# Kernel optimization log

Hardware: AMD Instinct MI355X
Metric: run time of the kernel (lower is better)

The kernel has to match this reference:

```python
import jax, jax.numpy as jnp
import numpy as np

B, S, D, H = 32, 128, 64, 4
HD = D // H            # head dim 16
HT = 4 * D             # hidden_t_dim = 256
TE = 4 * HT            # time_embed_dim = 1024
V = 1024               # vocab
STEP = 0.1             # step_size (Lie-Trotter step)


def setup_inputs():
    key = jax.random.key(0)
    ks = jax.random.split(key, 12)
    n = lambda k, shp: 0.02 * jax.random.normal(k, shp, jnp.float32)
    return dict(
        inputs_idx=jax.random.randint(ks[0], (B, S), 0, V),
        num_loops=100,
        wte=n(ks[1], (V, D)),
        wpe=n(ks[2], (S, D)),
        t_w1=n(ks[3], (HT, TE)), t_b1=jnp.zeros((TE,), jnp.float32),
        t_w2=n(ks[4], (TE, D)), t_b2=jnp.zeros((D,), jnp.float32),
        ln1_g=jnp.ones((D,), jnp.float32), ln1_b=jnp.zeros((D,), jnp.float32),
        w_qkv=n(ks[5], (D, 3 * D)), b_qkv=jnp.zeros((3 * D,), jnp.float32),
        w_o=n(ks[6], (D, D)), b_o=jnp.zeros((D,), jnp.float32),
        ln2_g=jnp.ones((D,), jnp.float32), ln2_b=jnp.zeros((D,), jnp.float32),
        w_fc=n(ks[7], (D, 4 * D)), b_fc=jnp.zeros((4 * D,), jnp.float32),
        w_pr=n(ks[8], (4 * D, D)), b_pr=jnp.zeros((D,), jnp.float32),
        lnf_g=jnp.ones((D,), jnp.float32), lnf_b=jnp.zeros((D,), jnp.float32),
    )


def _ln(x, g, b, eps=1e-5):
    mu = jnp.mean(x, axis=-1, keepdims=True)
    var = jnp.var(x, axis=-1, keepdims=True)
    return (x - mu) * jax.lax.rsqrt(var + eps) * g + b


def _timestep_embedding(t, dim):
    # sinusoidal (diffusion-style) embedding of scalar step index t -> (dim,)
    half = dim // 2
    freqs = jnp.exp(-np.log(10000.0) * jnp.arange(half, dtype=jnp.float32) / half)
    args = t * freqs
    return jnp.concatenate([jnp.cos(args), jnp.sin(args)], axis=-1)


def reference(inputs_idx, num_loops, wte, wpe, t_w1, t_b1, t_w2, t_b2,
              ln1_g, ln1_b, w_qkv, b_qkv, w_o, b_o,
              ln2_g, ln2_b, w_fc, b_fc, w_pr, b_pr, lnf_g, lnf_b):
    x = wte[inputs_idx] + wpe[jnp.arange(S)]          # (B,S,D)
    neg_inf = jnp.float32(-1e9)
    cmask = jnp.where(jnp.tril(jnp.ones((S, S), bool)), 0.0, neg_inf)  # causal
    scale = 1.0 / np.sqrt(HD)

    def step(x, t):
        # shared time embedding added to state each loop iteration
        te = _timestep_embedding(t, HT)
        temb = jax.nn.silu(te @ t_w1 + t_b1) @ t_w2 + t_b2   # (D,)
        x = x + temb
        # pre-norm attention, Lie-Trotter sub-step
        h = _ln(x, ln1_g, ln1_b)
        qkv = h @ w_qkv + b_qkv                               # (B,S,3D)
        q, k, v = jnp.split(qkv, 3, axis=-1)
        q = q.reshape(B, S, H, HD)
        k = k.reshape(B, S, H, HD)
        v = v.reshape(B, S, H, HD)
        att = jnp.einsum('bqhd,bkhd->bhqk', q, k) * scale + cmask
        att = jax.nn.softmax(att, axis=-1)
        a = jnp.einsum('bhqk,bkhd->bqhd', att, v).reshape(B, S, D)
        x = x + STEP * (a @ w_o + b_o)
        # pre-norm MLP, second sub-step
        h = _ln(x, ln2_g, ln2_b)
        m = jax.nn.gelu(h @ w_fc + b_fc) @ w_pr + b_pr
        x = x + STEP * m
        return x, None

    ts = jnp.arange(num_loops, dtype=jnp.float32)
    x, _ = jax.lax.scan(step, x, ts)
    return _ln(x, lnf_g, lnf_b)
```

## Files before the change

kernel.cpp:

```cpp
#include <hip/hip_runtime.h>
#include <hip/hip_bf16.h>
#include <math.h>

#define BB   32
#define SS   128
#define DD   64
#define HTT  256
#define TEE  1024
#define NTHR 1024
#define STEPF 0.1f

typedef __attribute__((ext_vector_type(8))) short short8b;
typedef __attribute__((ext_vector_type(4))) float float4v;

__device__ __forceinline__ unsigned short f2b(float f) {
    union { float f; unsigned int u; } x; x.f = f;
    unsigned int u = x.u + 0x7FFFu + ((x.u >> 16) & 1u);
    return (unsigned short)(u >> 16);
}
__device__ __forceinline__ unsigned int pack2(float lo, float hi) {
    return (unsigned int)f2b(lo) | ((unsigned int)f2b(hi) << 16);
}

__global__ void pack_frags(const float* __restrict__ w_qkv,
                           const float* __restrict__ w_o,
                           const float* __restrict__ w_fc,
                           const float* __restrict__ w_pr,
                           unsigned short* __restrict__ frags) {
    const int tile = blockIdx.x;
    const int t = threadIdx.x;
    const int lane = t >> 3, e = t & 7;
    const float* W; int N, nt, ks;
    if (tile < 24)      { W = w_qkv; N = 192; int s = tile;      nt = s >> 1; ks = s & 1; }
    else if (tile < 32) { W = w_o;   N = 64;  int s = tile - 24; nt = s >> 1; ks = s & 1; }
    else if (tile < 64) { W = w_fc;  N = 256; int s = tile - 32; nt = s >> 1; ks = s & 1; }
    else                { W = w_pr;  N = 64;  int s = tile - 64; nt = s >> 3; ks = s & 7; }
    const int k   = ks * 32 + (lane >> 4) * 8 + e;
    const int col = nt * 16 + (lane & 15);
    frags[tile * 512 + lane * 8 + e] = f2b(W[k * N + col]);
}

__global__ void temb_precompute(const int* __restrict__ nloops_p,
                                const float* __restrict__ t_w1,
                                const float* __restrict__ t_b1,
                                const float* __restrict__ t_w2,
                                const float* __restrict__ t_b2,
                                float* __restrict__ tembBuf) {
    const int t = blockIdx.x;
    const int nl = nloops_p[0];
    if (t >= nl) return;

    __shared__ float te_s[HTT];
    __shared__ float h1[TEE];
    const int tid = threadIdx.x;
    const float tf = (float)t;

    {
        int fi = (tid < 128) ? tid : (tid - 128);
        float freq = expf(-9.210340371976184f * (float)fi * (1.0f / 128.0f));
        float arg = tf * freq;
        te_s[tid] = (tid < 128) ? cosf(arg) : sinf(arg);
    }
    __syncthreads();

    for (int j = tid; j < TEE; j += 256) {
        float acc = t_b1[j];
        for (int i = 0; i < HTT; ++i)
            acc = fmaf(te_s[i], t_w1[i * TEE + j], acc);
        h1[j] = acc / (1.0f + expf(-acc));
    }
    __syncthreads();

    {
        const int d = tid >> 2, part = tid & 3;
        float acc = 0.0f;
        for (int j = part; j < TEE; j += 4)
            acc = fmaf(h1[j], t_w2[j * DD + d], acc);
        acc += __shfl_xor(acc, 1);
        acc += __shfl_xor(acc, 2);
        if (part == 0) tembBuf[t * DD + d] = acc + t_b2[d];
    }
}

__device__ __forceinline__ float gelu_tanh(float u) {
    float z = 0.7978845608028654f * (u + 0.044715f * u * u * u);
    float e = __expf(2.0f * z);
    float th = 1.0f - 2.0f / (e + 1.0f);
    return 0.5f * u * (1.0f + th);
}

__global__ __launch_bounds__(NTHR, 4)
void looped_tf(const int* __restrict__ idx,
               const int* __restrict__ nloops_p,
               const float* __restrict__ wte,
               const float* __restrict__ wpe,
               const float* __restrict__ ln1_g, const float* __restrict__ ln1_b,
               const float* __restrict__ b_qkv,
               const float* __restrict__ b_o,
               const float* __restrict__ ln2_g, const float* __restrict__ ln2_b,
               const float* __restrict__ b_fc,
               const float* __restrict__ b_pr,
               const float* __restrict__ lnf_g, const float* __restrict__ lnf_b,
               const float* __restrict__ tembBuf,
               const unsigned short* __restrict__ frags,
               float* __restrict__ out) {
    __shared__ __align__(16) unsigned short hsb[SS * DD];
    __shared__ __align__(16) unsigned char pool[66560];
    __shared__ __align__(16) unsigned char pstage[16 * 2 * 1152];
    __shared__ __align__(16) unsigned short wfrag[16384];
    __shared__ __align__(16) float2 lnred[SS][2];

    unsigned char* qb  = pool;
    unsigned char* kb  = pool + 24576;
    unsigned char* vtb = pool + 49152;
    unsigned short* msb = (unsigned short*)pool;

    const unsigned short* fcF = frags + 32 * 512;
    const unsigned short* prF = frags + 64 * 512;

    const int b   = blockIdx.x;
    const int tid = threadIdx.x;
    const int nl  = nloops_p[0];
    const int wv  = tid >> 6;
    const int wg  = wv & 7;
    const int wh  = wv >> 3;
    const int ln  = tid & 63;
    const int fr  = ln & 15;
    const int fq  = ln >> 4;
    const int rowbase = wg * 16 + fq * 4;

    for (int i = tid; i < 2048; i += NTHR)
        ((int4*)wfrag)[i] = ((const int4*)frags)[i];

    float bqkvr[6], bfcr[8], bor[2], bprr[2];
    float l1g[2], l1b[2], l2g[2], l2b[2], lfg[2], lfb[2];
#pragma unroll
    for (int i = 0; i < 6; ++i) bqkvr[i] = b_qkv[(wh * 6 + i) * 16 + fr];
#pragma unroll
    for (int i = 0; i < 8; ++i) bfcr[i] = b_fc[(wh * 8 + i) * 16 + fr];
#pragma unroll
    for (int nc = 0; nc < 2; ++nc) {
        int c = (wh * 2 + nc) * 16 + fr;
        bor[nc] = b_o[c];  bprr[nc] = b_pr[c];
        l1g[nc] = ln1_g[c]; l1b[nc] = ln1_b[c];
        l2g[nc] = ln2_g[c]; l2b[nc] = ln2_b[c];
        lfg[nc] = lnf_g[c]; lfb[nc] = lnf_b[c];
    }

    float xr[4][2];
#pragma unroll
    for (int r = 0; r < 4; ++r) {
        int row = rowbase + r;
        int iv = idx[b * SS + row];
#pragma unroll
        for (int nc = 0; nc < 2; ++nc) {
            int c = (wh * 2 + nc) * 16 + fr;
            xr[r][nc] = wte[iv * 64 + c] + wpe[row * 64 + c];
        }
    }
    __syncthreads();

    auto ln_fused = [&](const float* g2, const float* b2) {
        float s1[4], s2[4];
#pragma unroll
        for (int r = 0; r < 4; ++r) {
            s1[r] = xr[r][0] + xr[r][1];
            s2[r] = xr[r][0]*xr[r][0] + xr[r][1]*xr[r][1];
        }
#pragma unroll
        for (int m = 1; m <= 8; m <<= 1) {
#pragma unroll
            for (int r = 0; r < 4; ++r) {
                s1[r] += __shfl_xor(s1[r], m);
                s2[r] += __shfl_xor(s2[r], m);
            }
        }
        if (fr == 0) {
#pragma unroll
            for (int r = 0; r < 4; ++r) {
                float2 v; v.x = s1[r]; v.y = s2[r];
                lnred[rowbase + r][wh] = v;
            }
        }
        __syncthreads();
#pragma unroll
        for (int r = 0; r < 4; ++r) {
            float2 oth = lnred[rowbase + r][wh ^ 1];
            float t1 = s1[r] + oth.x, t2 = s2[r] + oth.y;
            float mu = t1 * (1.0f / 64.0f);
            float var = t2 * (1.0f / 64.0f) - mu * mu;
            float rs = rsqrtf(var + 1e-5f);
            int row = rowbase + r;
            int swz = (row & 7) << 4;
#pragma unroll
            for (int nc = 0; nc < 2; ++nc) {
                float h = (xr[r][nc] - mu) * rs * g2[nc] + b2[nc];
                int byte = (row * 128 + ((wh * 2 + nc) * 16 + fr) * 2) ^ swz;
                *(unsigned short*)((char*)hsb + byte) = f2b(h);
            }
        }
        __syncthreads();
    };

    auto load_afrag = [&](const unsigned short* buf, int rstrideB, int kstep) -> short8b {
        int row = wg * 16 + fr;
        int byte = row * rstrideB + kstep * 64 + fq * 16;
        return *(const short8b*)((const char*)buf + (byte ^ ((row & 7) << 4)));
    };

    if (nl > 0) {
#pragma unroll
        for (int nc = 0; nc < 2; ++nc) {
            float tv = tembBuf[(wh * 2 + nc) * 16 + fr];
#pragma unroll
            for (int r = 0; r < 4; ++r) xr[r][nc] += tv;
        }
        ln_fused(l1g, l1b);
    }

    for (int t = 0; t < nl; ++t) {
        {
            short8b a0 = load_afrag(hsb, 128, 0);
            short8b a1 = load_afrag(hsb, 128, 1);
            float4v acc[6];
#pragma unroll
            for (int i = 0; i < 6; ++i) acc[i] = (float4v)0.0f;
#pragma unroll
            for (int i = 0; i < 6; ++i) {
                int nt = wh * 6 + i;
                short8b b0 = *(const short8b*)(&wfrag[(nt * 2 + 0) * 512 + ln * 8]);
                short8b b1 = *(const short8b*)(&wfrag[(nt * 2 + 1) * 512 + ln * 8]);
                acc[i] = __builtin_amdgcn_mfma_f32_16x16x32_bf16(a0, b0, acc[i], 0, 0, 0);
                acc[i] = __builtin_amdgcn_mfma_f32_16x16x32_bf16(a1, b1, acc[i], 0, 0, 0);
            }
#pragma unroll
            for (int i = 0; i < 6; ++i) {
                int nt = wh * 6 + i;
#pragma unroll
                for (int r = 0; r < 4; ++r) {
                    int row = rowbase + r;
                    unsigned short bv = f2b(acc[i][r] + bqkvr[i]);
                    if (nt < 4) {
                        int byte = nt * 6144 + row * 48 + fr * 2;
                        byte ^= ((row >> 3) & 7) << 4;
                        *(unsigned short*)(qb + byte) = bv;
                    } else if (nt < 8) {
                        int h = nt - 4;
                        int p = (row >> 1) + 64 * (row & 1);
                        *(unsigned short*)(kb + h * 6144 + p * 48 + fr * 2) = bv;
                    } else {
                        int h = nt - 8;
                        *(unsigned short*)(vtb + h * 4352 + fr * 272 + row * 2) = bv;
                    }
                }
            }
        }
        __syncthreads();

        {
            const bool lo = (ln < 32);
            short8b aq[2];
#pragma unroll
            for (int hh = 0; hh < 2; ++hh) {
                int h = wh * 2 + hh;
                short8b z = (short8b)(short)0;
                if (lo) {
                    int q = wg + 8 * fr;
                    int byte = h * 6144 + q * 48 + (fq & 1) * 16;
                    byte ^= (fr & 7) << 4;
                    z = *(const short8b*)(qb + byte);
                }
                aq[hh] = z;
            }
            short8b onesb;
#pragma unroll
            for (int e = 0; e < 8; ++e) onesb[e] = (short)0x3F80;

            float4v o[2], lac[2];
#pragma unroll
            for (int hh = 0; hh < 2; ++hh) { o[hh] = (float4v)0.0f; lac[hh] = (float4v)0.0f; }

            for (int ktp = 0; ktp < 4; ++ktp) {
#pragma unroll
                for (int hh = 0; hh < 2; ++hh) {
                    int h = wh * 2 + hh;
                    unsigned char* pst = pstage + (wv * 2 + hh) * 1152;
                    short8b bk0 = (short8b)(short)0, bk1 = (short8b)(short)0;
                    if (lo) {
                        int kbase = h * 6144 + (fq & 1) * 16;
                        bk0 = *(const short8b*)(kb + kbase + (ktp * 16 + fr) * 48);
                        bk1 = *(const short8b*)(kb + kbase + (64 + ktp * 16 + fr) * 48);
                    }
                    float4v s0 = __builtin_amdgcn_mfma_f32_16x16x32_bf16(aq[hh], bk0, (float4v)0.0f, 0, 0, 0);
                    float4v s1 = __builtin_amdgcn_mfma_f32_16x16x32_bf16(aq[hh], bk1, (float4v)0.0f, 0, 0, 0);
#pragma unroll
                    for (int r = 0; r < 4; ++r) {
                        int j = 4 * fq + r;
                        int q = wg + 8 * j;
                        int k0 = ktp * 32 + 2 * fr;
                        float p0 = (k0     <= q) ? __expf(s0[r] * 0.25f) : 0.0f;
                        float p1 = (k0 + 1 <= q) ? __expf(s1[r] * 0.25f) : 0.0f;
                        *(unsigned int*)(pst + j * 72 + fr * 4) = pack2(p0, p1);
                    }
                    short8b ap = *(const short8b*)(pst + fr * 72 + fq * 16);
                    short8b bv = *(const short8b*)(vtb + h * 4352 + fr * 272 + ktp * 64 + fq * 16);
                    o[hh]   = __builtin_amdgcn_mfma_f32_16x16x32_bf16(ap, bv, o[hh], 0, 0, 0);
                    lac[hh] = __builtin_amdgcn_mfma_f32_16x16x32_bf16(ap, onesb, lac[hh], 0, 0, 0);
                }
            }
#pragma unroll
            for (int hh = 0; hh < 2; ++hh) {
                int h = wh * 2 + hh;
#pragma unroll
                for (int r = 0; r < 4; ++r) {
                    int j = 4 * fq + r;
                    int q = wg + 8 * j;
                    float val = o[hh][r] / lac[hh][r];
                    int byte = (q * 128 + (h * 16 + fr) * 2) ^ ((q & 7) << 4);
                    *(unsigned short*)((char*)hsb + byte) = f2b(val);
                }
            }
        }
        __syncthreads();

        {
            short8b a0 = load_afrag(hsb, 128, 0);
            short8b a1 = load_afrag(hsb, 128, 1);
            float4v acc[2];
#pragma unroll
            for (int i = 0; i < 2; ++i) acc[i] = (float4v)0.0f;
#pragma unroll
            for (int i = 0; i < 2; ++i) {
                int nt = wh * 2 + i;
                short8b b0 = *(const short8b*)(&wfrag[(24 + nt * 2 + 0) * 512 + ln * 8]);
                short8b b1 = *(const short8b*)(&wfrag[(24 + nt * 2 + 1) * 512 + ln * 8]);
                acc[i] = __builtin_amdgcn_mfma_f32_16x16x32_bf16(a0, b0, acc[i], 0, 0, 0);
                acc[i] = __builtin_amdgcn_mfma_f32_16x16x32_bf16(a1, b1, acc[i], 0, 0, 0);
            }
#pragma unroll
            for (int i = 0; i < 2; ++i)
#pragma unroll
                for (int r = 0; r < 4; ++r)
                    xr[r][i] += STEPF * (acc[i][r] + bor[i]);
            ln_fused(l2g, l2b);
        }

        {
            short8b a0 = load_afrag(hsb, 128, 0);
            short8b a1 = load_afrag(hsb, 128, 1);
            float4v acc[8];
#pragma unroll
            for (int i = 0; i < 8; ++i) acc[i] = (float4v)0.0f;
#pragma unroll
            for (int i = 0; i < 8; ++i) {
                int nt = wh * 8 + i;
                short8b b0 = *(const short8b*)(fcF + ((nt * 2 + 0) * 64 + ln) * 8);
                short8b b1 = *(const short8b*)(fcF + ((nt * 2 + 1) * 64 + ln) * 8);
                acc[i] = __builtin_amdgcn_mfma_f32_16x16x32_bf16(a0, b0, acc[i], 0, 0, 0);
                acc[i] = __builtin_amdgcn_mfma_f32_16x16x32_bf16(a1, b1, acc[i], 0, 0, 0);
            }
            char* base = (char*)msb;
#pragma unroll
            for (int i = 0; i < 8; ++i) {
                int nt = wh * 8 + i;
#pragma unroll
                for (int r = 0; r < 4; ++r) {
                    int row = rowbase + r;
                    int byte = row * 512 + (nt * 16 + fr) * 2;
                    *(unsigned short*)(base + (byte ^ ((row & 7) << 4))) =
                        f2b(gelu_tanh(acc[i][r] + bfcr[i]));
                }
            }
        }
        __syncthreads();

        {
            short8b am[8];
#pragma unroll
            for (int ks = 0; ks < 8; ++ks)
                am[ks] = load_afrag(msb, 512, ks);
            float4v acc[2];
#pragma unroll
            for (int i = 0; i < 2; ++i) acc[i] = (float4v)0.0f;
#pragma unroll
            for (int i = 0; i < 2; ++i) {
                int nt = wh * 2 + i;
#pragma unroll
                for (int ks = 0; ks < 8; ++ks) {
                    short8b bp = *(const short8b*)(prF + ((nt * 8 + ks) * 64 + ln) * 8);
                    acc[i] = __builtin_amdgcn_mfma_f32_16x16x32_bf16(am[ks], bp, acc[i], 0, 0, 0);
                }
            }
#pragma unroll
            for (int i = 0; i < 2; ++i)
#pragma unroll
                for (int r = 0; r < 4; ++r)
                    xr[r][i] += STEPF * (acc[i][r] + bprr[i]);

            if (t + 1 < nl) {
#pragma unroll
                for (int nc = 0; nc < 2; ++nc) {
                    float tv = tembBuf[(t + 1) * 64 + (wh * 2 + nc) * 16 + fr];
#pragma unroll
                    for (int r = 0; r < 4; ++r) xr[r][nc] += tv;
                }
                ln_fused(l1g, l1b);
            }
        }
    }

    {
        float s1[4], s2[4];
#pragma unroll
        for (int r = 0; r < 4; ++r) {
            s1[r] = xr[r][0] + xr[r][1];
            s2[r] = xr[r][0]*xr[r][0] + xr[r][1]*xr[r][1];
        }
#pragma unroll
        for (int m = 1; m <= 8; m <<= 1) {
#pragma unroll
            for (int r = 0; r < 4; ++r) {
                s1[r] += __shfl_xor(s1[r], m);
                s2[r] += __shfl_xor(s2[r], m);
            }
        }
        if (fr == 0) {
#pragma unroll
            for (int r = 0; r < 4; ++r) {
                float2 v; v.x = s1[r]; v.y = s2[r];
                lnred[rowbase + r][wh] = v;
            }
        }
        __syncthreads();
#pragma unroll
        for (int r = 0; r < 4; ++r) {
            float2 oth = lnred[rowbase + r][wh ^ 1];
            float t1 = s1[r] + oth.x, t2 = s2[r] + oth.y;
            float mu = t1 * (1.0f / 64.0f);
            float var = t2 * (1.0f / 64.0f) - mu * mu;
            float rs = rsqrtf(var + 1e-5f);
            int row = rowbase + r;
#pragma unroll
            for (int nc = 0; nc < 2; ++nc) {
                int c = (wh * 2 + nc) * 16 + fr;
                out[b * SS * DD + row * 64 + c] = (xr[r][nc] - mu) * rs * lfg[nc] + lfb[nc];
            }
        }
    }
}

extern "C" void kernel_launch(void* const* d_in, const int* in_sizes, int n_in,
                              void* d_out, int out_size, void* d_ws, size_t ws_size,
                              hipStream_t stream) {
    const int*   idx    = (const int*)  d_in[0];
    const int*   nloops = (const int*)  d_in[1];
    const float* wte    = (const float*)d_in[2];
    const float* wpe    = (const float*)d_in[3];
    const float* t_w1   = (const float*)d_in[4];
    const float* t_b1   = (const float*)d_in[5];
    const float* t_w2   = (const float*)d_in[6];
    const float* t_b2   = (const float*)d_in[7];
    const float* ln1_g  = (const float*)d_in[8];
    const float* ln1_b  = (const float*)d_in[9];
    const float* w_qkv  = (const float*)d_in[10];
    const float* b_qkv  = (const float*)d_in[11];
    const float* w_o    = (const float*)d_in[12];
    const float* b_o    = (const float*)d_in[13];
    const float* ln2_g  = (const float*)d_in[14];
    const float* ln2_b  = (const float*)d_in[15];
    const float* w_fc   = (const float*)d_in[16];
    const float* b_fc   = (const float*)d_in[17];
    const float* w_pr   = (const float*)d_in[18];
    const float* b_pr   = (const float*)d_in[19];
    const float* lnf_g  = (const float*)d_in[20];
    const float* lnf_b  = (const float*)d_in[21];

    float* tembBuf = (float*)d_ws;
    unsigned short* frags = (unsigned short*)((char*)d_ws + 32768);

    pack_frags<<<96, 512, 0, stream>>>(w_qkv, w_o, w_fc, w_pr, frags);
    temb_precompute<<<128, 256, 0, stream>>>(nloops, t_w1, t_b1, t_w2, t_b2, tembBuf);
    looped_tf<<<BB, NTHR, 0, stream>>>(idx, nloops, wte, wpe, ln1_g, ln1_b,
                                       b_qkv, b_o, ln2_g, ln2_b,
                                       b_fc, b_pr, lnf_g, lnf_b,
                                       tembBuf, frags, (float*)d_out);
}
```

Baseline: 3.504 ms.

## Interleave attention head MFMAs, prescale Q, and use hardware bf16 pack

Splits the per-head attention loop into three phases (all score MFMAs, then exp/pack, then PV MFMAs) so the two heads' MFMAs can overlap with the exp work. Folds the 1/sqrt(hd) scale into Q when it is written as bf16, removing a multiply per score. Replaces the software bf16 round-and-pack with the v_cvt_pk_bf16_f32 instruction and pins waves_per_eu to 4. This adds register pressure from holding both heads' scores at once.

```diff
diff --git a/kernel.cpp b/kernel.cpp
--- a/kernel.cpp
+++ b/kernel.cpp
@@ -18,8 +18,10 @@
     unsigned int u = x.u + 0x7FFFu + ((x.u >> 16) & 1u);
     return (unsigned short)(u >> 16);
 }
-__device__ __forceinline__ unsigned int pack2(float lo, float hi) {
-    return (unsigned int)f2b(lo) | ((unsigned int)f2b(hi) << 16);
+__device__ __forceinline__ unsigned int cvtpk2(float lo, float hi) {
+    unsigned int r;
+    asm("v_cvt_pk_bf16_f32 %0, %1, %2" : "=v"(r) : "v"(lo), "v"(hi));
+    return r;
 }
 
 __global__ void pack_frags(const float* __restrict__ w_qkv,
@@ -89,7 +91,7 @@
     return 0.5f * u * (1.0f + th);
 }
 
-__global__ __launch_bounds__(NTHR, 4)
+__global__ __launch_bounds__(NTHR, 4) __attribute__((amdgpu_waves_per_eu(4, 4)))
 void looped_tf(const int* __restrict__ idx,
                const int* __restrict__ nloops_p,
                const float* __restrict__ wte,
@@ -239,18 +241,19 @@
 #pragma unroll
                 for (int r = 0; r < 4; ++r) {
                     int row = rowbase + r;
-                    unsigned short bv = f2b(acc[i][r] + bqkvr[i]);
+                    float v = acc[i][r] + bqkvr[i];
                     if (nt < 4) {
+                        unsigned short bv = f2b(v * 0.25f);
                         int byte = nt * 6144 + row * 48 + fr * 2;
                         byte ^= ((row >> 3) & 7) << 4;
                         *(unsigned short*)(qb + byte) = bv;
                     } else if (nt < 8) {
                         int h = nt - 4;
                         int p = (row >> 1) + 64 * (row & 1);
-                        *(unsigned short*)(kb + h * 6144 + p * 48 + fr * 2) = bv;
+                        *(unsigned short*)(kb + h * 6144 + p * 48 + fr * 2) = f2b(v);
                     } else {
                         int h = nt - 8;
-                        *(unsigned short*)(vtb + h * 4352 + fr * 272 + row * 2) = bv;
+                        *(unsigned short*)(vtb + h * 4352 + fr * 272 + row * 2) = f2b(v);
                     }
                 }
             }
@@ -281,27 +284,36 @@
             for (int hh = 0; hh < 2; ++hh) { o[hh] = (float4v)0.0f; lac[hh] = (float4v)0.0f; }
 
             for (int ktp = 0; ktp < 4; ++ktp) {
+                float4v s0h[2], s1h[2];
 #pragma unroll
                 for (int hh = 0; hh < 2; ++hh) {
                     int h = wh * 2 + hh;
-                    unsigned char* pst = pstage + (wv * 2 + hh) * 1152;
                     short8b bk0 = (short8b)(short)0, bk1 = (short8b)(short)0;
                     if (lo) {
                         int kbase = h * 6144 + (fq & 1) * 16;
                         bk0 = *(const short8b*)(kb + kbase + (ktp * 16 + fr) * 48);
                         bk1 = *(const short8b*)(kb + kbase + (64 + ktp * 16 + fr) * 48);
                     }
-                    float4v s0 = __builtin_amdgcn_mfma_f32_16x16x32_bf16(aq[hh], bk0, (float4v)0.0f, 0, 0, 0);
-                    float4v s1 = __builtin_amdgcn_mfma_f32_16x16x32_bf16(aq[hh], bk1, (float4v)0.0f, 0, 0, 0);
+                    s0h[hh] = __builtin_amdgcn_mfma_f32_16x16x32_bf16(aq[hh], bk0, (float4v)0.0f, 0, 0, 0);
+                    s1h[hh] = __builtin_amdgcn_mfma_f32_16x16x32_bf16(aq[hh], bk1, (float4v)0.0f, 0, 0, 0);
+                }
+#pragma unroll
+                for (int hh = 0; hh < 2; ++hh) {
+                    unsigned char* pst = pstage + (wv * 2 + hh) * 1152;
 #pragma unroll
                     for (int r = 0; r < 4; ++r) {
                         int j = 4 * fq + r;
                         int q = wg + 8 * j;
                         int k0 = ktp * 32 + 2 * fr;
-                        float p0 = (k0     <= q) ? __expf(s0[r] * 0.25f) : 0.0f;
-                        float p1 = (k0 + 1 <= q) ? __expf(s1[r] * 0.25f) : 0.0f;
-                        *(unsigned int*)(pst + j * 72 + fr * 4) = pack2(p0, p1);
+                        float p0 = (k0     <= q) ? __expf(s0h[hh][r]) : 0.0f;
+                        float p1 = (k0 + 1 <= q) ? __expf(s1h[hh][r]) : 0.0f;
+                        *(unsigned int*)(pst + j * 72 + fr * 4) = cvtpk2(p0, p1);
                     }
+                }
+#pragma unroll
+                for (int hh = 0; hh < 2; ++hh) {
+                    int h = wh * 2 + hh;
+                    unsigned char* pst = pstage + (wv * 2 + hh) * 1152;
                     short8b ap = *(const short8b*)(pst + fr * 72 + fq * 16);
                     short8b bv = *(const short8b*)(vtb + h * 4352 + fr * 272 + ktp * 64 + fq * 16);
                     o[hh]   = __builtin_amdgcn_mfma_f32_16x16x32_bf16(ap, bv, o[hh], 0, 0, 0);
```

New measurement: 3.239 ms. -7.6%, faster.
